# Kernel tuning notes

Hardware: AMD Instinct MI355X
Metric: run time of the kernel (lower is better)

The kernel has to match this reference:

```python
import jax, jax.numpy as jnp
import numpy as np

N = 500000      # examples = M * (nr+1)
K = 20          # context set size (indices[:, 3:])
NR = 24         # negatives per positive
H = 128         # hidden_channels == node feature dim
NODES = 10000   # ingredient vocabulary


def setup_inputs() -> dict:
    key = jax.random.key(0)
    ks = jax.random.split(key, 6)
    indices = jax.random.randint(ks[0], (N, 3 + K), 0, NODES)
    x = jax.random.normal(ks[1], (NODES, H), dtype=jnp.float32)
    scale = 0.02
    W1 = jax.random.normal(ks[2], (H, 3 * H), dtype=jnp.float32) * scale
    b1 = jnp.zeros((H,), jnp.float32)
    W2 = jax.random.normal(ks[3], (H // 2, H), dtype=jnp.float32) * scale
    b2 = jnp.zeros((H // 2,), jnp.float32)
    W3 = jax.random.normal(ks[4], (1, H // 2), dtype=jnp.float32) * scale
    b3 = jnp.zeros((1,), jnp.float32)
    return {"indices": indices, "nr": NR, "x": x,
            "W1": W1, "b1": b1, "W2": W2, "b2": b2, "W3": W3, "b3": b3}


def _embed_context(ctx_idx, x, nr):
    # ctx_idx: [N, K]; one context row per group of (nr+1) examples
    new_idx = ctx_idx[:-1:nr + 1]                 # [M, K]
    emb = x[new_idx]                               # [M, K, H] gather
    s = emb.sum(axis=1)                            # [M, H]
    norm = jnp.maximum((new_idx > 0).sum(axis=1), 1).astype(x.dtype)[:, None]
    mean = s / norm                                # masked mean over context
    return jnp.repeat(mean, nr + 1, axis=0)        # broadcast back to [N, H]


def reference(indices, nr, x, W1, b1, W2, b2, W3, b3):
    ing1 = x[indices[:, 0]]                        # [N, H]
    ing2 = x[indices[:, 1]]                        # [N, H]
    set_emb = _embed_context(indices[:, 3:], x, nr)  # [N, H]
    y = jnp.concatenate([ing1, ing2, set_emb], axis=1)  # [N, 3H]
    y = jax.nn.relu(y @ W1.T + b1)
    y = jax.nn.relu(y @ W2.T + b2)
    return y @ W3.T + b3                           # [N, 1]
```

## Files before the change

kernel.cpp:

```cpp
#include <hip/hip_runtime.h>
#include <hip/hip_bf16.h>

#define N_ROWS   500000
#define NR1      25
#define NGROUPS  20000
#define KCTX     20
#define H        128
#define NODES    10000
#define IDX_COLS 23

typedef __attribute__((ext_vector_type(8))) short short8;
typedef __attribute__((ext_vector_type(4))) float f32x4;

__device__ __forceinline__ unsigned pkbf(float lo, float hi) {
  __hip_bfloat162 h = __float22bfloat162_rn(make_float2(lo, hi));
  union { __hip_bfloat162 h; unsigned u; } c; c.h = h;
  return c.u;
}
__device__ __forceinline__ float lo2f(unsigned u) {
  union { unsigned u; float f; } c; c.u = u << 16; return c.f;
}
__device__ __forceinline__ float hi2f(unsigned u) {
  union { unsigned u; float f; } c; c.u = u & 0xffff0000u; return c.f;
}

#define PN 64
#define PBLK      ((NODES + PN - 1) / PN)
#define B_FAT     ((NGROUPS + 63) / 64)
#define B_P12     B_FAT
#define B_IDX     (B_P12 + 4 * PBLK)
#define IDX_ROWS  256
#define IDX_BLKS  ((N_ROWS + IDX_ROWS - 1) / IDX_ROWS)
#define B_W2FP    (B_IDX + IDX_BLKS)
#define PRE_BLOCKS (B_W2FP + 1)

__global__ __launch_bounds__(256) void k_pre(
    const int* __restrict__ indices, const float* __restrict__ x,
    const float* __restrict__ W1, const float* __restrict__ b1,
    const float* __restrict__ W2,
    unsigned short* __restrict__ Pb, unsigned short* __restrict__ Pgb,
    unsigned short* __restrict__ w2f, int2* __restrict__ idx2) {
  __shared__ __align__(16) short lds_all[16384];

  const int tid = threadIdx.x;
  const int bid = blockIdx.x;
  const int lane = tid & 63;
  const int wvid = tid >> 6;
  const int col  = lane & 15;
  const int quad = lane >> 4;

  if (bid >= B_IDX) {
    if (bid == B_W2FP) {
#pragma unroll
      for (int i = 0; i < 4; ++i) {
        const int fi = i * 4 + wvid;
        const int kt = fi >> 2, ct = fi & 3;
        const float* __restrict__ src =
            W2 + (size_t)(ct * 16 + col) * H + kt * 32 + quad * 8;
        const float4 v0 = *(const float4*)src;
        const float4 v1 = *(const float4*)(src + 4);
        union { short8 v; unsigned u[4]; } pk;
        pk.u[0] = pkbf(v0.x, v0.y);
        pk.u[1] = pkbf(v0.z, v0.w);
        pk.u[2] = pkbf(v1.x, v1.y);
        pk.u[3] = pkbf(v1.z, v1.w);
        *(short8*)(w2f + (size_t)(fi * 64 + lane) * 8) = pk.v;
      }
      return;
    }
    int* ilds = (int*)lds_all;
    const int rbase = (bid - B_IDX) * IDX_ROWS;
    const int nrows = (N_ROWS - rbase < IDX_ROWS) ? (N_ROWS - rbase) : IDX_ROWS;
    const int nints = nrows * IDX_COLS;
    const int* __restrict__ src = indices + (size_t)rbase * IDX_COLS;
    const int n4 = nints >> 2;
    const int4* __restrict__ src4 = (const int4*)src;
    for (int i = tid; i < n4; i += 256) ((int4*)ilds)[i] = src4[i];
    for (int i = (n4 << 2) + tid; i < nints; i += 256) ilds[i] = src[i];
    __syncthreads();
    for (int r = tid; r < nrows; r += 256)
      idx2[rbase + r] = make_int2(ilds[r * IDX_COLS], ilds[r * IDX_COLS + 1]);
    return;
  }

  if (bid < B_FAT) {
    short* w13h = lds_all;
    short* mlds = lds_all + 8192;
    const int gbase = bid * 64;

    const int jj = lane * 2;
#pragma unroll
    for (int it = 0; it < 8; ++it) {
      const int ga = gbase + wvid * 16 + it;
      const int gb = ga + 8;
      const int gac = (ga < NGROUPS) ? ga : (NGROUPS - 1);
      const int gbc = (gb < NGROUPS) ? gb : (NGROUPS - 1);
      const int* __restrict__ ra = indices + (size_t)gac * NR1 * IDX_COLS + 3;
      const int* __restrict__ rb = indices + (size_t)gbc * NR1 * IDX_COLS + 3;
      float a0 = 0.f, a1 = 0.f, c0 = 0.f, c1 = 0.f;
      int ca = 0, cb = 0;
#pragma unroll
      for (int c = 0; c < KCTX; ++c) {
        const int ia = ra[c], ib = rb[c];
        const float2 va = *(const float2*)(x + (size_t)ia * H + jj);
        const float2 vb = *(const float2*)(x + (size_t)ib * H + jj);
        a0 += va.x; a1 += va.y; c0 += vb.x; c1 += vb.y;
        ca += (ia > 0) ? 1 : 0; cb += (ib > 0) ? 1 : 0;
      }
      const float rna = 1.f / (float)((ca > 1) ? ca : 1);
      const float rnb = 1.f / (float)((cb > 1) ? cb : 1);
      {
        const int row = wvid * 16 + it;
        const int sb = row * 128 + (((lane >> 2) ^ (row & 7)) << 3) + (lane & 3) * 2;
        *(unsigned*)&mlds[sb] = pkbf(a0 * rna, a1 * rna);
      }
      {
        const int row = wvid * 16 + it + 8;
        const int sb = row * 128 + (((lane >> 2) ^ (row & 7)) << 3) + (lane & 3) * 2;
        *(unsigned*)&mlds[sb] = pkbf(c0 * rnb, c1 * rnb);
      }
    }

#pragma unroll
    for (int it = 0; it < 8; ++it) {
      const int f  = it * 256 + tid;
      const int j  = f >> 5;
      const int q4 = f & 31;
      const float4 v = *(const float4*)(W1 + (size_t)j * (3 * H) + 2 * H + q4 * 4);
      const int sidx = j * 128 + (((q4 >> 1) ^ (j & 7)) << 3) + (q4 & 1) * 4;
      *(unsigned*)&w13h[sidx]     = pkbf(v.x, v.y);
      *(unsigned*)&w13h[sidx + 2] = pkbf(v.z, v.w);
    }
    __syncthreads();

    short8 Af[4];
    const int arow = wvid * 16 + col;
#pragma unroll
    for (int kt = 0; kt < 4; ++kt)
      Af[kt] = *(const short8*)
          &mlds[arow * 128 + (((kt * 4 + quad) ^ (arow & 7)) << 3)];

    for (int ch = 0; ch < 2; ++ch) {
      if (ch == 1) {
        __syncthreads();
#pragma unroll
        for (int it = 0; it < 8; ++it) {
          const int f  = it * 256 + tid;
          const int j  = f >> 5;
          const int q4 = f & 31;
          const float4 v =
              *(const float4*)(W1 + (size_t)(64 + j) * (3 * H) + 2 * H + q4 * 4);
          const int sidx = j * 128 + (((q4 >> 1) ^ (j & 7)) << 3) + (q4 & 1) * 4;
          *(unsigned*)&w13h[sidx]     = pkbf(v.x, v.y);
          *(unsigned*)&w13h[sidx + 2] = pkbf(v.z, v.w);
        }
        __syncthreads();
      }
      f32x4 acc[4];
#pragma unroll
      for (int ct = 0; ct < 4; ++ct) acc[ct] = (f32x4)(0.f);
#pragma unroll
      for (int kt = 0; kt < 4; ++kt) {
#pragma unroll
        for (int ct = 0; ct < 4; ++ct) {
          const int brow = ct * 16 + col;
          const short8 Bf = *(const short8*)
              &w13h[brow * 128 + (((kt * 4 + quad) ^ (brow & 7)) << 3)];
          acc[ct] = __builtin_amdgcn_mfma_f32_16x16x32_bf16(Af[kt], Bf, acc[ct], 0, 0, 0);
        }
      }
      float b1v[4];
#pragma unroll
      for (int ct = 0; ct < 4; ++ct) b1v[ct] = b1[ch * 64 + ct * 16 + col];
#pragma unroll
      for (int reg = 0; reg < 4; ++reg) {
        const int g2 = gbase + wvid * 16 + quad * 4 + reg;
        if (g2 < NGROUPS) {
#pragma unroll
          for (int ct = 0; ct < 4; ++ct) {
            union { unsigned u; unsigned short s[2]; } cc;
            cc.u = pkbf(acc[ct][reg] + b1v[ct], 0.f);
            Pgb[(size_t)g2 * H + ch * 64 + ct * 16 + col] = cc.s[0];
          }
        }
      }
    }
    return;
  }

  {
    short* wlds = lds_all;
    const int local = bid - B_P12;
    const int m   = local / (2 * PBLK);
    const int sub = local - m * (2 * PBLK);
    const int tbase = (sub >> 1) * PN;
    const int ch    = sub & 1;

#pragma unroll
    for (int it = 0; it < 8; ++it) {
      const int f  = it * 256 + tid;
      const int j  = f >> 5;
      const int q4 = f & 31;
      const float4 v =
          *(const float4*)(W1 + (size_t)(ch * 64 + j) * (3 * H) + m * H + q4 * 4);
      const int sidx = j * 128 + (((q4 >> 1) ^ (j & 7)) << 3) + (q4 & 1) * 4;
      *(unsigned*)&wlds[sidx]     = pkbf(v.x, v.y);
      *(unsigned*)&wlds[sidx + 2] = pkbf(v.z, v.w);
    }
    __syncthreads();

    int node = tbase + wvid * 16 + col;
    if (node > NODES - 1) node = NODES - 1;
    const float4* __restrict__ xr = (const float4*)(x + (size_t)node * H);
    short8 Af[4];
#pragma unroll
    for (int kt = 0; kt < 4; ++kt) {
      const int f4 = kt * 8 + quad * 2;
      const float4 v0 = xr[f4], v1 = xr[f4 + 1];
      union { short8 v; unsigned u[4]; } pk;
      pk.u[0] = pkbf(v0.x, v0.y);
      pk.u[1] = pkbf(v0.z, v0.w);
      pk.u[2] = pkbf(v1.x, v1.y);
      pk.u[3] = pkbf(v1.z, v1.w);
      Af[kt] = pk.v;
    }

    f32x4 acc[4];
#pragma unroll
    for (int ct = 0; ct < 4; ++ct) acc[ct] = (f32x4)(0.f);
#pragma unroll
    for (int kt = 0; kt < 4; ++kt) {
#pragma unroll
      for (int ct = 0; ct < 4; ++ct) {
        const int brow = ct * 16 + col;
        const short8 Bf = *(const short8*)
            &wlds[brow * 128 + (((kt * 4 + quad) ^ (brow & 7)) << 3)];
        acc[ct] = __builtin_amdgcn_mfma_f32_16x16x32_bf16(Af[kt], Bf, acc[ct], 0, 0, 0);
      }
    }

    unsigned short* __restrict__ Pm = Pb + (size_t)m * NODES * H;
#pragma unroll
    for (int reg = 0; reg < 4; ++reg) {
      const int n = tbase + wvid * 16 + quad * 4 + reg;
      if (n < NODES) {
#pragma unroll
        for (int ct = 0; ct < 4; ++ct) {
          union { unsigned u; unsigned short s[2]; } c;
          c.u = pkbf(acc[ct][reg], 0.f);
          Pm[(size_t)n * H + ch * 64 + ct * 16 + col] = c.s[0];
        }
      }
    }
  }
}

#define RPW 32
__global__ __launch_bounds__(256, 4) void k_main(
    const int2* __restrict__ idx2,
    const unsigned short* __restrict__ P1b, const unsigned short* __restrict__ P2b,
    const unsigned short* __restrict__ Pgb, const unsigned short* __restrict__ w2f,
    const float* __restrict__ b2, const float* __restrict__ W3,
    const float* __restrict__ b3, float* __restrict__ out) {
  __shared__ __align__(16) short w2s[16 * 64 * 8];

  const int tid  = threadIdx.x;
  const int lane = tid & 63;
  const int wv   = tid >> 6;
  const int col  = lane & 15;
  const int quad = lane >> 4;

  {
    const short8* __restrict__ src = (const short8*)w2f;
    short8* dst = (short8*)w2s;
#pragma unroll
    for (int i = 0; i < 4; ++i) dst[i * 256 + tid] = src[i * 256 + tid];
  }
  __syncthreads();

  const int Rw = (blockIdx.x * 4 + wv) * RPW;
  const int r0 = Rw + col, r1 = Rw + 16 + col;
  const int rc0 = (r0 < N_ROWS) ? r0 : (N_ROWS - 1);
  const int rc1 = (r1 < N_ROWS) ? r1 : (N_ROWS - 1);
  const int g0 = rc0 / NR1, g1 = rc1 / NR1;

  const short8* __restrict__ pc0 = (const short8*)(Pgb + (size_t)g0 * H);
  const short8* __restrict__ pc1 = (const short8*)(Pgb + (size_t)g1 * H);
  short8 uc0[4], uc1[4];
#pragma unroll
  for (int kt = 0; kt < 4; ++kt) {
    uc0[kt] = pc0[kt * 4 + quad];
    uc1[kt] = pc1[kt * 4 + quad];
  }

  const int2 iA = idx2[rc0];
  const int2 iB = idx2[rc1];

  const short8* __restrict__ pa0 = (const short8*)(P1b + (size_t)iA.x * H);
  const short8* __restrict__ pb0 = (const short8*)(P2b + (size_t)iA.y * H);
  const short8* __restrict__ pa1 = (const short8*)(P1b + (size_t)iB.x * H);
  const short8* __restrict__ pb1 = (const short8*)(P2b + (size_t)iB.y * H);
  short8 ua0[4], ub0[4], ua1[4], ub1[4];
#pragma unroll
  for (int kt = 0; kt < 4; ++kt) {
    ua0[kt] = pa0[kt * 4 + quad];
    ub0[kt] = pb0[kt * 4 + quad];
    ua1[kt] = pa1[kt * 4 + quad];
    ub1[kt] = pb1[kt * 4 + quad];
  }
  __builtin_amdgcn_sched_barrier(0);

  float b2v[4], w3v[4];
#pragma unroll
  for (int ct = 0; ct < 4; ++ct) {
    b2v[ct] = b2[ct * 16 + col];
    w3v[ct] = W3[ct * 16 + col];
  }
  const float bias3 = b3[0];

  short8 A0[4], A1[4];
#pragma unroll
  for (int kt = 0; kt < 4; ++kt) {
    union { short8 v; unsigned u[4]; } va, vb, vc;
    va.v = ua0[kt]; vb.v = ub0[kt]; vc.v = uc0[kt];
    union { short8 v; unsigned u[4]; } pk;
#pragma unroll
    for (int w = 0; w < 4; ++w) {
      const float hl = fmaxf(lo2f(va.u[w]) + lo2f(vb.u[w]) + lo2f(vc.u[w]), 0.f);
      const float hh = fmaxf(hi2f(va.u[w]) + hi2f(vb.u[w]) + hi2f(vc.u[w]), 0.f);
      pk.u[w] = pkbf(hl, hh);
    }
    A0[kt] = pk.v;
  }
#pragma unroll
  for (int kt = 0; kt < 4; ++kt) {
    union { short8 v; unsigned u[4]; } va, vb, vc;
    va.v = ua1[kt]; vb.v = ub1[kt]; vc.v = uc1[kt];
    union { short8 v; unsigned u[4]; } pk;
#pragma unroll
    for (int w = 0; w < 4; ++w) {
      const float hl = fmaxf(lo2f(va.u[w]) + lo2f(vb.u[w]) + lo2f(vc.u[w]), 0.f);
      const float hh = fmaxf(hi2f(va.u[w]) + hi2f(vb.u[w]) + hi2f(vc.u[w]), 0.f);
      pk.u[w] = pkbf(hl, hh);
    }
    A1[kt] = pk.v;
  }

  f32x4 acc0[4], acc1[4];
#pragma unroll
  for (int ct = 0; ct < 4; ++ct) { acc0[ct] = (f32x4)(0.f); acc1[ct] = (f32x4)(0.f); }
#pragma unroll
  for (int kt = 0; kt < 4; ++kt) {
#pragma unroll
    for (int ct = 0; ct < 4; ++ct) {
      const short8 Bf = *(const short8*)&w2s[((kt * 4 + ct) * 64 + lane) * 8];
      acc0[ct] = __builtin_amdgcn_mfma_f32_16x16x32_bf16(A0[kt], Bf, acc0[ct], 0, 0, 0);
      acc1[ct] = __builtin_amdgcn_mfma_f32_16x16x32_bf16(A1[kt], Bf, acc1[ct], 0, 0, 0);
    }
  }

#pragma unroll
  for (int grp = 0; grp < 2; ++grp) {
#pragma unroll
    for (int reg = 0; reg < 4; ++reg) {
      float s = 0.f;
#pragma unroll
      for (int ct = 0; ct < 4; ++ct) {
        const float a = (grp == 0) ? acc0[ct][reg] : acc1[ct][reg];
        s += fmaxf(a + b2v[ct], 0.f) * w3v[ct];
      }
      s += __shfl_xor(s, 1);
      s += __shfl_xor(s, 2);
      s += __shfl_xor(s, 4);
      s += __shfl_xor(s, 8);
      if (col == 0) {
        const int row = Rw + grp * 16 + quad * 4 + reg;
        if (row < N_ROWS) out[row] = s + bias3;
      }
    }
  }
}

extern "C" void kernel_launch(void* const* d_in, const int* in_sizes, int n_in,
                              void* d_out, int out_size, void* d_ws, size_t ws_size,
                              hipStream_t stream) {
  const int*   indices = (const int*)  d_in[0];
  const float* x  = (const float*)d_in[2];
  const float* W1 = (const float*)d_in[3];
  const float* b1 = (const float*)d_in[4];
  const float* W2 = (const float*)d_in[5];
  const float* b2 = (const float*)d_in[6];
  const float* W3 = (const float*)d_in[7];
  const float* b3 = (const float*)d_in[8];
  float* out = (float*)d_out;

  unsigned short* Pb  = (unsigned short*)d_ws;
  unsigned short* P1b = Pb;
  unsigned short* P2b = Pb + (size_t)NODES * H;
  unsigned short* Pgb = Pb + (size_t)2 * NODES * H;
  unsigned short* w2f = Pgb + (size_t)NGROUPS * H;
  int2* idx2 = (int2*)(w2f + 16 * 64 * 8);

  k_pre<<<PRE_BLOCKS, 256, 0, stream>>>(indices, x, W1, b1, W2,
                                        Pb, Pgb, w2f, idx2);
  k_main<<<(N_ROWS + 4 * RPW - 1) / (4 * RPW), 256, 0, stream>>>(
      idx2, P1b, P2b, Pgb, w2f, b2, W3, b3, out);
}
```

Measured before the change: 165.4 us.

## Make main kernel persistent with software-pipelined gather prefetch

Replaces the one-shot-per-wave launch (32 rows per wave, about 3900 blocks) with a persistent grid of 1024 blocks. Each wave grid-strides over 16-row chunks and prefetches the next chunk's projected rows plus the index pair two chunks ahead while the current chunk is computed. The aim is to hide gather latency behind the MFMA work and to amortise the per-block LDS load of W2. The cost is fewer independent waves to hide latency with, and the fixed block count of 1024 may not fill the GPU evenly.

```diff
diff --git a/kernel.cpp b/kernel.cpp
--- a/kernel.cpp
+++ b/kernel.cpp
@@ -255,7 +255,8 @@
   }
 }
 
-#define RPW 32
+#define MAIN_BLOCKS 1024
+#define NCHUNK      (N_ROWS / 16)
 __global__ __launch_bounds__(256, 4) void k_main(
     const int2* __restrict__ idx2,
     const unsigned short* __restrict__ P1b, const unsigned short* __restrict__ P2b,
@@ -270,6 +271,28 @@
   const int col  = lane & 15;
   const int quad = lane >> 4;
 
+  const int NW   = MAIN_BLOCKS * 4;
+  const int wgid = blockIdx.x * 4 + wv;
+
+  short8 ua[4], ub[4], uc[4];
+  int2 iiN;
+  {
+    const int r = wgid * 16 + col;
+    const int2 ii = idx2[r];
+    const int g  = r / NR1;
+    const short8* __restrict__ pa = (const short8*)(P1b + (size_t)ii.x * H);
+    const short8* __restrict__ pb = (const short8*)(P2b + (size_t)ii.y * H);
+    const short8* __restrict__ pc = (const short8*)(Pgb + (size_t)g * H);
+#pragma unroll
+    for (int kt = 0; kt < 4; ++kt) {
+      ua[kt] = pa[kt * 4 + quad];
+      ub[kt] = pb[kt * 4 + quad];
+      uc[kt] = pc[kt * 4 + quad];
+    }
+    const int c1 = (wgid + NW < NCHUNK) ? (wgid + NW) : (NCHUNK - 1);
+    iiN = idx2[c1 * 16 + col];
+  }
+
   {
     const short8* __restrict__ src = (const short8*)w2f;
     short8* dst = (short8*)w2s;
@@ -278,38 +301,6 @@
   }
   __syncthreads();
 
-  const int Rw = (blockIdx.x * 4 + wv) * RPW;
-  const int r0 = Rw + col, r1 = Rw + 16 + col;
-  const int rc0 = (r0 < N_ROWS) ? r0 : (N_ROWS - 1);
-  const int rc1 = (r1 < N_ROWS) ? r1 : (N_ROWS - 1);
-  const int g0 = rc0 / NR1, g1 = rc1 / NR1;
-
-  const short8* __restrict__ pc0 = (const short8*)(Pgb + (size_t)g0 * H);
-  const short8* __restrict__ pc1 = (const short8*)(Pgb + (size_t)g1 * H);
-  short8 uc0[4], uc1[4];
-#pragma unroll
-  for (int kt = 0; kt < 4; ++kt) {
-    uc0[kt] = pc0[kt * 4 + quad];
-    uc1[kt] = pc1[kt * 4 + quad];
-  }
-
-  const int2 iA = idx2[rc0];
-  const int2 iB = idx2[rc1];
-
-  const short8* __restrict__ pa0 = (const short8*)(P1b + (size_t)iA.x * H);
-  const short8* __restrict__ pb0 = (const short8*)(P2b + (size_t)iA.y * H);
-  const short8* __restrict__ pa1 = (const short8*)(P1b + (size_t)iB.x * H);
-  const short8* __restrict__ pb1 = (const short8*)(P2b + (size_t)iB.y * H);
-  short8 ua0[4], ub0[4], ua1[4], ub1[4];
-#pragma unroll
-  for (int kt = 0; kt < 4; ++kt) {
-    ua0[kt] = pa0[kt * 4 + quad];
-    ub0[kt] = pb0[kt * 4 + quad];
-    ua1[kt] = pa1[kt * 4 + quad];
-    ub1[kt] = pb1[kt * 4 + quad];
-  }
-  __builtin_amdgcn_sched_barrier(0);
-
   float b2v[4], w3v[4];
 #pragma unroll
   for (int ct = 0; ct < 4; ++ct) {
@@ -318,66 +309,66 @@
   }
   const float bias3 = b3[0];
 
-  short8 A0[4], A1[4];
-#pragma unroll
-  for (int kt = 0; kt < 4; ++kt) {
-    union { short8 v; unsigned u[4]; } va, vb, vc;
-    va.v = ua0[kt]; vb.v = ub0[kt]; vc.v = uc0[kt];
-    union { short8 v; unsigned u[4]; } pk;
-#pragma unroll
-    for (int w = 0; w < 4; ++w) {
-      const float hl = fmaxf(lo2f(va.u[w]) + lo2f(vb.u[w]) + lo2f(vc.u[w]), 0.f);
-      const float hh = fmaxf(hi2f(va.u[w]) + hi2f(vb.u[w]) + hi2f(vc.u[w]), 0.f);
-      pk.u[w] = pkbf(hl, hh);
-    }
-    A0[kt] = pk.v;
-  }
-#pragma unroll
-  for (int kt = 0; kt < 4; ++kt) {
-    union { short8 v; unsigned u[4]; } va, vb, vc;
-    va.v = ua1[kt]; vb.v = ub1[kt]; vc.v = uc1[kt];
-    union { short8 v; unsigned u[4]; } pk;
-#pragma unroll
-    for (int w = 0; w < 4; ++w) {
-      const float hl = fmaxf(lo2f(va.u[w]) + lo2f(vb.u[w]) + lo2f(vc.u[w]), 0.f);
-      const float hh = fmaxf(hi2f(va.u[w]) + hi2f(vb.u[w]) + hi2f(vc.u[w]), 0.f);
-      pk.u[w] = pkbf(hl, hh);
-    }
-    A1[kt] = pk.v;
-  }
-
-  f32x4 acc0[4], acc1[4];
-#pragma unroll
-  for (int ct = 0; ct < 4; ++ct) { acc0[ct] = (f32x4)(0.f); acc1[ct] = (f32x4)(0.f); }
-#pragma unroll
-  for (int kt = 0; kt < 4; ++kt) {
-#pragma unroll
-    for (int ct = 0; ct < 4; ++ct) {
-      const short8 Bf = *(const short8*)&w2s[((kt * 4 + ct) * 64 + lane) * 8];
-      acc0[ct] = __builtin_amdgcn_mfma_f32_16x16x32_bf16(A0[kt], Bf, acc0[ct], 0, 0, 0);
-      acc1[ct] = __builtin_amdgcn_mfma_f32_16x16x32_bf16(A1[kt], Bf, acc1[ct], 0, 0, 0);
-    }
-  }
-
-#pragma unroll
-  for (int grp = 0; grp < 2; ++grp) {
+  for (int c = wgid; c < NCHUNK; c += NW) {
+    const int cNN = (c + 2 * NW < NCHUNK) ? (c + 2 * NW) : (NCHUNK - 1);
+    const int2 iiNN = idx2[cNN * 16 + col];
+
+    short8 A[4];
+#pragma unroll
+    for (int kt = 0; kt < 4; ++kt) {
+      union { short8 v; unsigned u[4]; } va, vb, vc;
+      va.v = ua[kt]; vb.v = ub[kt]; vc.v = uc[kt];
+      union { short8 v; unsigned u[4]; } pk;
+#pragma unroll
+      for (int w = 0; w < 4; ++w) {
+        const float hl = fmaxf(lo2f(va.u[w]) + lo2f(vb.u[w]) + lo2f(vc.u[w]), 0.f);
+        const float hh = fmaxf(hi2f(va.u[w]) + hi2f(vb.u[w]) + hi2f(vc.u[w]), 0.f);
+        pk.u[w] = pkbf(hl, hh);
+      }
+      A[kt] = pk.v;
+    }
+
+    {
+      const int cN = (c + NW < NCHUNK) ? (c + NW) : (NCHUNK - 1);
+      const int rN = cN * 16 + col;
+      const int gN = rN / NR1;
+      const short8* __restrict__ pa = (const short8*)(P1b + (size_t)iiN.x * H);
+      const short8* __restrict__ pb = (const short8*)(P2b + (size_t)iiN.y * H);
+      const short8* __restrict__ pc = (const short8*)(Pgb + (size_t)gN * H);
+#pragma unroll
+      for (int kt = 0; kt < 4; ++kt) {
+        ua[kt] = pa[kt * 4 + quad];
+        ub[kt] = pb[kt * 4 + quad];
+        uc[kt] = pc[kt * 4 + quad];
+      }
+    }
+    __builtin_amdgcn_sched_barrier(0);
+
+    f32x4 acc[4];
+#pragma unroll
+    for (int ct = 0; ct < 4; ++ct) acc[ct] = (f32x4)(0.f);
+#pragma unroll
+    for (int kt = 0; kt < 4; ++kt) {
+#pragma unroll
+      for (int ct = 0; ct < 4; ++ct) {
+        const short8 Bf = *(const short8*)&w2s[((kt * 4 + ct) * 64 + lane) * 8];
+        acc[ct] = __builtin_amdgcn_mfma_f32_16x16x32_bf16(A[kt], Bf, acc[ct], 0, 0, 0);
+      }
+    }
 #pragma unroll
     for (int reg = 0; reg < 4; ++reg) {
       float s = 0.f;
 #pragma unroll
-      for (int ct = 0; ct < 4; ++ct) {
-        const float a = (grp == 0) ? acc0[ct][reg] : acc1[ct][reg];
-        s += fmaxf(a + b2v[ct], 0.f) * w3v[ct];
-      }
+      for (int ct = 0; ct < 4; ++ct)
+        s += fmaxf(acc[ct][reg] + b2v[ct], 0.f) * w3v[ct];
       s += __shfl_xor(s, 1);
       s += __shfl_xor(s, 2);
       s += __shfl_xor(s, 4);
       s += __shfl_xor(s, 8);
-      if (col == 0) {
-        const int row = Rw + grp * 16 + quad * 4 + reg;
-        if (row < N_ROWS) out[row] = s + bias3;
-      }
-    }
+      if (col == 0) out[c * 16 + quad * 4 + reg] = s + bias3;
+    }
+
+    iiN = iiNN;
   }
 }
 
@@ -403,6 +394,6 @@
 
   k_pre<<<PRE_BLOCKS, 256, 0, stream>>>(indices, x, W1, b1, W2,
                                         Pb, Pgb, w2f, idx2);
-  k_main<<<(N_ROWS + 4 * RPW - 1) / (4 * RPW), 256, 0, stream>>>(
-      idx2, P1b, P2b, Pgb, w2f, b2, W3, b3, out);
-}
+  k_main<<<MAIN_BLOCKS, 256, 0, stream>>>(idx2, P1b, P2b, Pgb, w2f,
+                                          b2, W3, b3, out);
+}
```

Result: no change. 167.9 us (+1.5%).
